# Performance work log

Hardware: AMD Instinct MI355X
Metric: run time of the kernel (lower is better)

## Reference

```python
import jax, jax.numpy as jnp
import numpy as np
from jax import lax


def _xavier(key, shape):
    fan_out, fan_in = shape
    lim = float(np.sqrt(6.0 / (fan_in + fan_out)))
    return jax.random.uniform(key, shape, jnp.float32, -lim, lim)


def setup_inputs() -> dict:
    V, E, H, F, B = 32000, 512, 256, 256, 64
    key = jax.random.key(0)
    ks = jax.random.split(key, 16)
    emb = _xavier(ks[0], (V, E)).at[0].set(0.0)  # padding_idx=0 zeroed
    return {
        'enc_feat': jax.random.normal(ks[1], (B, F), jnp.float32),
        'emb': emb,
        'Wh': _xavier(ks[2], (H, F)), 'bh': jnp.zeros((H,), jnp.float32),
        'Wc': _xavier(ks[3], (H, F)), 'bc': jnp.zeros((H,), jnp.float32),
        'Wih0': _xavier(ks[4], (4 * H, E)), 'Whh0': _xavier(ks[5], (4 * H, H)),
        'bih0': jnp.zeros((4 * H,), jnp.float32), 'bhh0': jnp.zeros((4 * H,), jnp.float32),
        'Wih1': _xavier(ks[6], (4 * H, H)), 'Whh1': _xavier(ks[7], (4 * H, H)),
        'bih1': jnp.zeros((4 * H,), jnp.float32), 'bhh1': jnp.zeros((4 * H,), jnp.float32),
        'Wout': _xavier(ks[8], (V, H)), 'bout': jnp.zeros((V,), jnp.float32),
        'sos_id': 1, 'eos_id': 2, 'max_len': 48,
    }


def _lstm_cell(x, h, c, Wih, Whh, bih, bhh):
    # PyTorch gate order: i, f, g, o
    g = x @ Wih.T + h @ Whh.T + (bih + bhh)
    i, f, gg, o = jnp.split(g, 4, axis=-1)
    c_new = jax.nn.sigmoid(f) * c + jax.nn.sigmoid(i) * jnp.tanh(gg)
    h_new = jax.nn.sigmoid(o) * jnp.tanh(c_new)
    return h_new, c_new


def reference(enc_feat, emb, Wh, bh, Wc, bc, Wih0, Whh0, bih0, bhh0,
              Wih1, Whh1, bih1, bhh1, Wout, bout, sos_id, eos_id, max_len):
    B = enc_feat.shape[0]
    h_init = enc_feat @ Wh.T + bh  # [B, H], repeated over num_layers
    c_init = enc_feat @ Wc.T + bc
    tok0 = jnp.full((B,), sos_id, jnp.int32)
    carry0 = (tok0, h_init, c_init, h_init, c_init,
              jnp.zeros((B,), bool), jnp.array(False))

    def step(carry, _):
        tok, h0, c0, h1, c1, done, all_done = carry
        x = emb[tok]                                   # [B, E]
        h0, c0 = _lstm_cell(x, h0, c0, Wih0, Whh0, bih0, bhh0)
        h1, c1 = _lstm_cell(h0, h1, c1, Wih1, Whh1, bih1, bhh1)
        logits = h1 @ Wout.T + bout                    # [B, V]
        nt = jnp.argmax(logits, axis=-1).astype(jnp.int32)  # greedy decode
        out = jnp.where(all_done, 0, nt)               # torch pads with 0 after break
        done = done | (out == eos_id)
        all_done = all_done | jnp.all(done)
        return (out, h0, c0, h1, c1, done, all_done), out

    _, toks = lax.scan(step, carry0, None, length=max_len)  # [max_len, B]
    return toks.T.astype(jnp.int64)  # [B, max_len]
```

## Files before the change

### kernel.cpp

```cpp
#include <hip/hip_runtime.h>
#include <math.h>

#define TSTEPS 48
#define NCELL 32
#define ND 224
#define NBLK (NCELL + ND)

#define OFF_W0T   0
#define OFF_W1T   524288
#define OFF_WH0T  786432
#define OFF_WH1T  1048576
#define OFF_BS0   1310720
#define OFF_BS1   1311744
#define OFF_HINIT 1312768
#define OFF_CINIT 1329152
#define OFF_H0BUF 1345536
#define OFF_H1BUF 1361920
#define OFF_FLOAT_END 1378304

#define FSTR 32
#define FL_H0F   0
#define FL_H1C   1024
#define FL_H1ALL 2048
#define FL_DFLAG 3072
#define FL_DMIR  10240
#define FL_TOK   11264
#define NFLAGU32 12288

typedef float f4v __attribute__((ext_vector_type(4)));

__device__ __forceinline__ unsigned ld_cohu(const unsigned* p) {
  return __hip_atomic_load((unsigned*)p, __ATOMIC_RELAXED, __HIP_MEMORY_SCOPE_AGENT);
}
__device__ __forceinline__ void st_cohu(unsigned* p, unsigned v) {
  __hip_atomic_store(p, v, __ATOMIC_RELAXED, __HIP_MEMORY_SCOPE_AGENT);
}
__device__ __forceinline__ unsigned long long ld_coh64(const unsigned long long* p) {
  return __hip_atomic_load((unsigned long long*)p, __ATOMIC_RELAXED, __HIP_MEMORY_SCOPE_AGENT);
}
__device__ __forceinline__ void st_coh64(unsigned long long* p, unsigned long long v) {
  __hip_atomic_store(p, v, __ATOMIC_RELAXED, __HIP_MEMORY_SCOPE_AGENT);
}
__device__ __forceinline__ float4 ldg_coh_f4(const float4* p) {
  f4v r;
  asm volatile("global_load_dwordx4 %0, %1, off sc0 sc1\n\ts_waitcnt vmcnt(0)"
               : "=v"(r) : "v"(p) : "memory");
  return make_float4(r.x, r.y, r.z, r.w);
}
__device__ __forceinline__ void ldg_coh_f4x4(const float4* p0, const float4* p1,
                                             const float4* p2, const float4* p3,
                                             float4& a, float4& b, float4& c, float4& d) {
  f4v ra, rb, rc, rd;
  asm volatile(
      "global_load_dwordx4 %0, %4, off sc0 sc1\n\t"
      "global_load_dwordx4 %1, %5, off sc0 sc1\n\t"
      "global_load_dwordx4 %2, %6, off sc0 sc1\n\t"
      "global_load_dwordx4 %3, %7, off sc0 sc1\n\t"
      "s_waitcnt vmcnt(0)"
      : "=&v"(ra), "=&v"(rb), "=&v"(rc), "=&v"(rd)
      : "v"(p0), "v"(p1), "v"(p2), "v"(p3) : "memory");
  a = make_float4(ra.x, ra.y, ra.z, ra.w);
  b = make_float4(rb.x, rb.y, rb.z, rb.w);
  c = make_float4(rc.x, rc.y, rc.z, rc.w);
  d = make_float4(rd.x, rd.y, rd.z, rd.w);
}
__device__ __forceinline__ void stg_coh_f4(float4* p, float4 v) {
  f4v t = {v.x, v.y, v.z, v.w};
  asm volatile("global_store_dwordx4 %0, %1, off sc0 sc1" :: "v"(p), "v"(t) : "memory");
}
__device__ __forceinline__ void drain_vm() {
  asm volatile("s_waitcnt vmcnt(0)" ::: "memory");
}
__device__ __forceinline__ float4 ldnt_f4(const float4* p) {
  f4v v = __builtin_nontemporal_load((const f4v*)p);
  return make_float4(v.x, v.y, v.z, v.w);
}
__device__ __forceinline__ float sigf(float x) { return 1.0f / (1.0f + expf(-x)); }
__device__ __forceinline__ unsigned long long u64max(unsigned long long a, unsigned long long b) {
  return a > b ? a : b;
}
__device__ __forceinline__ unsigned long long wmax64(unsigned long long k) {
#pragma unroll
  for (int off = 1; off < 64; off <<= 1) {
    unsigned long long o = __shfl_xor(k, off, 64);
    k = u64max(k, o);
  }
  return k;
}
__device__ __forceinline__ unsigned long long packkey(float lg, int v) {
  unsigned u = __float_as_uint(lg);
  u = (u & 0x80000000u) ? ~u : (u | 0x80000000u);
  return ((unsigned long long)u << 32) | (unsigned)(~(unsigned)v);
}
__device__ __forceinline__ float4 f4add(float4 a, float4 b) {
  return make_float4(a.x + b.x, a.y + b.y, a.z + b.z, a.w + b.w);
}

__global__ void lstm_init_kernel(const float* enc, const float* Wh, const float* bh,
                                 const float* Wc, const float* bc,
                                 const float* bih0, const float* bhh0,
                                 const float* bih1, const float* bhh1,
                                 float* ws, unsigned long long* key2, unsigned* flags) {
  const int tid = threadIdx.x, blk = blockIdx.x;
  if (blk < 64) {
    __shared__ float el[256];
    el[tid] = enc[blk * 256 + tid];
    __syncthreads();
    const float4* el4 = (const float4*)el;
    const float4* wh4 = (const float4*)(Wh + tid * 256);
    const float4* wc4 = (const float4*)(Wc + tid * 256);
    float ah = bh[tid], ac = bc[tid];
#pragma unroll 4
    for (int f = 0; f < 64; ++f) {
      float4 x = el4[f], a = wh4[f], b = wc4[f];
      ah = fmaf(a.x, x.x, fmaf(a.y, x.y, fmaf(a.z, x.z, fmaf(a.w, x.w, ah))));
      ac = fmaf(b.x, x.x, fmaf(b.y, x.y, fmaf(b.z, x.z, fmaf(b.w, x.w, ac))));
    }
    ws[OFF_HINIT + blk * 256 + tid] = ah;
    ws[OFF_CINIT + blk * 256 + tid] = ac;
  } else if (blk == 64) {
    for (int g = tid; g < 1024; g += 256) {
      int hh = g >> 9, gc = g & 511;
      int row = (gc >> 7) * 256 + hh * 128 + (gc & 127);
      ws[OFF_BS0 + g] = bih0[row] + bhh0[row];
      ws[OFF_BS1 + g] = bih1[row] + bhh1[row];
    }
  } else {
    const int base = (blk - 65) * 256 + tid;
    for (int i = base; i < 64 * 256; i += 15 * 256) key2[i] = 0ull;
    for (int i = base; i < NFLAGU32; i += 15 * 256) flags[i] = 0u;
  }
}

__global__ void lstm_relayout_kernel(const float* Wih0, const float* Whh0,
                                     const float* Wih1, const float* Whh1, float* ws) {
  const int gid = blockIdx.x * 256 + threadIdx.x;
  const int gstr = 256 * 256;
  const float* srcs[4] = {Wih0, Wih1, Whh0, Whh1};
  const int dsts[4] = {OFF_W0T, OFF_W1T, OFF_WH0T, OFF_WH1T};
  const int k4tot[4] = {128, 64, 64, 64};
  for (int s = 0; s < 4; ++s) {
    const int n = 2 * k4tot[s] * 512;
    float4* dst = (float4*)(ws + dsts[s]);
    const float4* src = (const float4*)srcs[s];
    for (int e = gid; e < n; e += gstr) {
      int hh = e / (k4tot[s] * 512);
      int r = e - hh * k4tot[s] * 512;
      int k4 = r / 512, gc = r - k4 * 512;
      int row = (gc >> 7) * 256 + hh * 128 + (gc & 127);
      dst[e] = src[(size_t)row * k4tot[s] + k4];
    }
  }
}

struct CellSm {
  float x[4 * 512];
  float4 part[1024];
  float4 r0res[512];
  float4 r1res[512];
  float h0[4 * 256];
  float h1[4 * 256];
  float c0[4 * 128];
  float c1[4 * 128];
  int tok[4];
  unsigned fm[32];
  unsigned long long fred[16];
  int done4;
  int alldone;
};
struct DSm {
  float w[16 * 144 * 4];
  float h[64 * 68];
  unsigned long long kr[128];
  unsigned long long epi[16 * 64];
};
union Smem { CellSm c; DSm d; };

template <int K4H>
__device__ __forceinline__ void gemv_half(const float4* __restrict__ W,
                                          const float* __restrict__ xl, int xstride,
                                          float4* __restrict__ part, int tid) {
  const int kh = tid >> 9;
  float a0 = 0.f, a1 = 0.f, a2 = 0.f, a3 = 0.f;
  const float4* wp = W + (size_t)(kh * K4H) * 512 + (tid & 511);
  const float* x0 = xl + kh * K4H * 4;
#pragma unroll 8
  for (int i = 0; i < K4H; ++i) {
    float4 w = wp[(size_t)i * 512];
    float4 xa = *(const float4*)(x0 + i * 4);
    float4 xb = *(const float4*)(x0 + xstride + i * 4);
    float4 xc = *(const float4*)(x0 + 2 * xstride + i * 4);
    float4 xd = *(const float4*)(x0 + 3 * xstride + i * 4);
    a0 = fmaf(w.x, xa.x, fmaf(w.y, xa.y, fmaf(w.z, xa.z, fmaf(w.w, xa.w, a0))));
    a1 = fmaf(w.x, xb.x, fmaf(w.y, xb.y, fmaf(w.z, xb.z, fmaf(w.w, xb.w, a1))));
    a2 = fmaf(w.x, xc.x, fmaf(w.y, xc.y, fmaf(w.z, xc.z, fmaf(w.w, xc.w, a2))));
    a3 = fmaf(w.x, xd.x, fmaf(w.y, xd.y, fmaf(w.z, xd.z, fmaf(w.w, xd.w, a3))));
  }
  part[tid] = make_float4(a0, a1, a2, a3);
}

__device__ __forceinline__ void cellfold(const float4* part, const float4* rres,
                                         const float* bs, float* cst, float* hst,
                                         int hh, int tid) {
  if (tid < 512) {
    int jj = tid & 127, b = tid >> 7;
    float g[4];
#pragma unroll
    for (int q = 0; q < 4; ++q) {
      int gc = q * 128 + jj;
      g[q] = ((const float*)&part[gc])[b] + ((const float*)&part[512 + gc])[b] +
             ((const float*)&rres[gc])[b] + bs[gc];
    }
    float c = cst[b * 128 + jj];
    float cn = sigf(g[1]) * c + sigf(g[0]) * tanhf(g[2]);
    float hn = sigf(g[3]) * tanhf(cn);
    cst[b * 128 + jj] = cn;
    hst[b * 256 + hh * 128 + jj] = hn;
  }
}

__global__ __launch_bounds__(1024, 4) void lstm_decode_kernel(
    const float* __restrict__ emb, const float* __restrict__ Wout,
    const float* __restrict__ bout, const int* __restrict__ sosp,
    const int* __restrict__ eosp, float* __restrict__ ws,
    unsigned long long* __restrict__ key2, unsigned* __restrict__ flags,
    int* __restrict__ out) {
  const int tid = threadIdx.x;
  const int blk = blockIdx.x;
  __shared__ Smem sm;
  const int eos = *eosp;
  const int sos = *sosp;
  float4* h0b4 = (float4*)(ws + OFF_H0BUF);
  float4* h1b4 = (float4*)(ws + OFF_H1BUF);

  if (blk < NCELL) {
    const int bg = blk >> 1, hh = blk & 1, ph = 1 - hh;
    const float4* W0 = (const float4*)(ws + OFF_W0T) + (size_t)hh * 128 * 512;
    const float4* W1 = (const float4*)(ws + OFF_W1T) + (size_t)hh * 64 * 512;
    const float4* WH0 = (const float4*)(ws + OFF_WH0T) + (size_t)hh * 64 * 512;
    const float4* WH1 = (const float4*)(ws + OFF_WH1T) + (size_t)hh * 64 * 512;
    const float* bs0 = ws + OFF_BS0 + hh * 512;
    const float* bs1 = ws + OFF_BS1 + hh * 512;

    {
      int b = tid >> 8, k = tid & 255;
      float hv = ws[OFF_HINIT + (bg * 4 + b) * 256 + k];
      sm.c.h0[b * 256 + k] = hv;
      sm.c.h1[b * 256 + k] = hv;
    }
    if (tid < 512) {
      int b = tid >> 7, jj = tid & 127;
      float cv = ws[OFF_CINIT + (bg * 4 + b) * 256 + hh * 128 + jj];
      sm.c.c0[b * 128 + jj] = cv;
      sm.c.c1[b * 128 + jj] = cv;
    }
    if (tid < 4) sm.c.tok[tid] = sos;
    if (tid == 0) { sm.c.done4 = 0; sm.c.alldone = 0; }
    __syncthreads();
    gemv_half<32>(WH0, sm.c.h0, 256, sm.c.part, tid);
    __syncthreads();
    if (tid < 512) sm.c.r0res[tid] = f4add(sm.c.part[tid], sm.c.part[512 + tid]);
    __syncthreads();
    gemv_half<32>(WH1, sm.c.h1, 256, sm.c.part, tid);
    __syncthreads();
    if (tid < 512) sm.c.r1res[tid] = f4add(sm.c.part[tid], sm.c.part[512 + tid]);
    __syncthreads();

    for (int t = 0; t < TSTEPS; ++t) {
      const unsigned T = (unsigned)(t + 1);
      if (tid < 512) {
        int b = tid >> 7, j = tid & 127;
        ((float4*)sm.c.x)[b * 128 + j] = ((const float4*)emb)[(size_t)sm.c.tok[b] * 128 + j];
      }
      __syncthreads();
      gemv_half<64>(W0, sm.c.x, 512, sm.c.part, tid);
      __syncthreads();
      cellfold(sm.c.part, sm.c.r0res, bs0, sm.c.c0, sm.c.h0, hh, tid);
      __syncthreads();
      if (tid < 128) {
        int b = tid >> 5, j = tid & 31;
        float4 v = *(float4*)&sm.c.h0[b * 256 + hh * 128 + j * 4];
        stg_coh_f4(h0b4 + (bg * 4 + b) * 64 + hh * 32 + j, v);
      }
      drain_vm();
      __syncthreads();
      if (tid == 0) {
        st_cohu(flags + FL_H0F + blk * FSTR, T);
        while (ld_cohu(flags + FL_H0F + (blk ^ 1) * FSTR) < T) __builtin_amdgcn_s_sleep(1);
      }
      __syncthreads();
      if (tid < 128) {
        int b = tid >> 5, j = tid & 31;
        float4 v = ldg_coh_f4(h0b4 + (bg * 4 + b) * 64 + ph * 32 + j);
        *(float4*)&sm.c.h0[b * 256 + ph * 128 + j * 4] = v;
      }
      __syncthreads();
      gemv_half<32>(W1, sm.c.h0, 256, sm.c.part, tid);
      __syncthreads();
      cellfold(sm.c.part, sm.c.r1res, bs1, sm.c.c1, sm.c.h1, hh, tid);
      __syncthreads();
      if (tid < 128) {
        int b = tid >> 5, j = tid & 31;
        float4 v = *(float4*)&sm.c.h1[b * 256 + hh * 128 + j * 4];
        stg_coh_f4(h1b4 + (bg * 4 + b) * 64 + hh * 32 + j, v);
      }
      drain_vm();
      __syncthreads();
      if (tid == 0) {
        st_cohu(flags + FL_H1C + blk * FSTR, T);
        while (ld_cohu(flags + FL_H1C + (blk ^ 1) * FSTR) < T) __builtin_amdgcn_s_sleep(1);
      }
      __syncthreads();
      if (tid < 128) {
        int b = tid >> 5, j = tid & 31;
        float4 v = ldg_coh_f4(h1b4 + (bg * 4 + b) * 64 + ph * 32 + j);
        *(float4*)&sm.c.h1[b * 256 + ph * 128 + j * 4] = v;
      }
      __syncthreads();
      if (t > 0) {
        if (tid < 64) {
          unsigned tgt = (unsigned)t << 8;
          unsigned got = tgt;
          for (;;) {
            if (tid < 32) got = ld_cohu(flags + FL_TOK + tid * FSTR);
            if (__all((int)(got >= tgt))) break;
            __builtin_amdgcn_s_sleep(2);
          }
          if (tid < 32) sm.c.fm[tid] = got & 0xFFu;
        }
        __syncthreads();
        if (tid < 64) {
          int ok = 1;
          if (tid < 32) ok = (sm.c.fm[tid] == 0xFu);
          int all = __all(ok);
          if (tid == 0) sm.c.alldone = all;
        }
        __syncthreads();
      }
      gemv_half<32>(WH0, sm.c.h0, 256, sm.c.part, tid);
      __syncthreads();
      if (tid < 512) sm.c.r0res[tid] = f4add(sm.c.part[tid], sm.c.part[512 + tid]);
      __syncthreads();
      gemv_half<32>(WH1, sm.c.h1, 256, sm.c.part, tid);
      __syncthreads();
      if (tid < 512) sm.c.r1res[tid] = f4add(sm.c.part[tid], sm.c.part[512 + tid]);
      __syncthreads();
      if (tid < 64) {
        unsigned v = T;
        for (;;) {
          if (tid < 7) v = ld_cohu(flags + FL_DFLAG + (blk * 7 + tid) * FSTR);
          if (__all((int)(v >= T))) break;
          __builtin_amdgcn_s_sleep(4);
        }
      }
      __syncthreads();
      if (tid == 0) st_cohu(flags + FL_DMIR + blk * FSTR, T);
      if (tid < 64) {
        unsigned v = T;
        for (;;) {
          if (tid < 32) v = ld_cohu(flags + FL_DMIR + tid * FSTR);
          if (__all((int)(v >= T))) break;
          __builtin_amdgcn_s_sleep(2);
        }
      }
      __syncthreads();
      {
        int bb = tid >> 8, i = tid & 255;
        unsigned long long k = ld_coh64(key2 + (size_t)(bg * 4 + bb) * 256 + i);
        k = wmax64(k);
        if ((tid & 63) == 0) sm.c.fred[tid >> 6] = k;
      }
      __syncthreads();
      if (tid < 4) {
        int bb = tid;
        unsigned long long m = u64max(u64max(sm.c.fred[bb * 4], sm.c.fred[bb * 4 + 1]),
                                      u64max(sm.c.fred[bb * 4 + 2], sm.c.fred[bb * 4 + 3]));
        int v = (int)(~(unsigned)m);
        int outv = sm.c.alldone ? 0 : v;
        out[(bg * 4 + bb) * TSTEPS + t] = outv;
        int nd = ((sm.c.done4 >> bb) & 1) | (outv == eos ? 1 : 0);
        sm.c.tok[bb] = outv;
        sm.c.fm[bb] = (unsigned)nd;
      }
      __syncthreads();
      if (tid == 0) {
        int mask = (int)(sm.c.fm[0] | (sm.c.fm[1] << 1) | (sm.c.fm[2] << 2) | (sm.c.fm[3] << 3));
        sm.c.done4 = mask;
        if (t < TSTEPS - 1)
          st_cohu(flags + FL_TOK + blk * FSTR, ((unsigned)(t + 1) << 8) | (unsigned)mask);
      }
      __syncthreads();
    }
  } else {
    const int d = blk - NCELL;
    const int r0 = (d * 32000) / ND, r1 = ((d + 1) * 32000) / ND;
    const int rows = r1 - r0, nep = rows - 128;
    const int bg = tid >> 7, v = tid & 127;
    const int erow = tid >> 6, eb = tid & 63;
    const float4* Wout4 = (const float4*)Wout;
    const int nq = 144 * 16;

    for (int t = 0; t < TSTEPS; ++t) {
      const unsigned T = (unsigned)(t + 1);
      float4 wpre[3];
#pragma unroll
      for (int p = 0; p < 3; ++p) {
        int e = tid + p * 1024;
        if (e < nq) {
          int j = e / 144, r = e - j * 144;
          int rc = r0 + r; if (rc > 31999) rc = 31999;
          wpre[p] = ldnt_f4(Wout4 + (size_t)rc * 64 + j);
        } else wpre[p] = make_float4(0.f, 0.f, 0.f, 0.f);
      }
#pragma unroll
      for (int p = 0; p < 3; ++p) {
        int e = tid + p * 1024;
        if (e < nq) {
          int j = e / 144, r = e - j * 144;
          *(float4*)&sm.d.w[(j * 144 + r) * 4] = wpre[p];
        }
      }
      if (tid < 64) {
        unsigned hv = T;
        for (;;) {
          if (tid < 32) hv = ld_cohu(flags + FL_H1C + tid * FSTR);
          if (__all((int)(hv >= T))) break;
          __builtin_amdgcn_s_sleep(4);
        }
      }
      __syncthreads();
      float4 hpre[4];
      {
        int b = tid >> 4, j = tid & 15;
        const float4* hp = (const float4*)h1b4 + (size_t)b * 64 + j;
        ldg_coh_f4x4(hp, hp + 16, hp + 32, hp + 48, hpre[0], hpre[1], hpre[2], hpre[3]);
      }
      float acc[8];
#pragma unroll
      for (int i = 0; i < 8; ++i) acc[i] = 0.f;
      float eacc = 0.f;

      for (int kc = 0; kc < 4; ++kc) {
        if (kc > 0) {
          __syncthreads();
#pragma unroll
          for (int p = 0; p < 3; ++p) {
            int e = tid + p * 1024;
            if (e < nq) {
              int j = e / 144, r = e - j * 144;
              *(float4*)&sm.d.w[(j * 144 + r) * 4] = wpre[p];
            }
          }
        }
        {
          int b = tid >> 4, j = tid & 15;
          *(float4*)&sm.d.h[b * 68 + j * 4] = hpre[kc];
        }
        __syncthreads();
        if (kc < 3) {
#pragma unroll
          for (int p = 0; p < 3; ++p) {
            int e = tid + p * 1024;
            if (e < nq) {
              int j = e / 144, r = e - j * 144;
              int rc = r0 + r; if (rc > 31999) rc = 31999;
              wpre[p] = ldnt_f4(Wout4 + (size_t)rc * 64 + (kc + 1) * 16 + j);
            }
          }
        }
#pragma unroll 4
        for (int k4 = 0; k4 < 16; ++k4) {
          float4 w4 = *(const float4*)&sm.d.w[(k4 * 144 + v) * 4];
#pragma unroll
          for (int bi = 0; bi < 8; ++bi) {
            float4 h4 = *(const float4*)&sm.d.h[(bg * 8 + bi) * 68 + k4 * 4];
            acc[bi] = fmaf(w4.x, h4.x, fmaf(w4.y, h4.y, fmaf(w4.z, h4.z, fmaf(w4.w, h4.w, acc[bi]))));
          }
        }
        if (erow < nep) {
#pragma unroll 4
          for (int k4 = 0; k4 < 16; ++k4) {
            float4 w4 = *(const float4*)&sm.d.w[(k4 * 144 + 128 + erow) * 4];
            float4 h4 = *(const float4*)&sm.d.h[eb * 68 + k4 * 4];
            eacc = fmaf(w4.x, h4.x, fmaf(w4.y, h4.y, fmaf(w4.z, h4.z, fmaf(w4.w, h4.w, eacc))));
          }
        }
      }
      {
        float bb_ = bout[r0 + v];
#pragma unroll
        for (int bi = 0; bi < 8; ++bi) {
          unsigned long long k = packkey(acc[bi] + bb_, r0 + v);
          k = wmax64(k);
          if ((tid & 63) == 0) sm.d.kr[(bg * 8 + bi) * 2 + (v >> 6)] = k;
        }
      }
      if (erow < nep) {
        sm.d.epi[erow * 64 + eb] = packkey(eacc + bout[r0 + 128 + erow], r0 + 128 + erow);
      } else {
        sm.d.epi[erow * 64 + eb] = 0ull;
      }
      __syncthreads();
      if (tid < 64) {
        unsigned long long m = u64max(sm.d.kr[tid * 2], sm.d.kr[tid * 2 + 1]);
#pragma unroll
        for (int er = 0; er < 15; ++er) m = u64max(m, sm.d.epi[er * 64 + tid]);
        st_coh64(key2 + (size_t)tid * 256 + d, m);
      }
      drain_vm();
      __syncthreads();
      if (tid == 0) st_cohu(flags + FL_DFLAG + d * FSTR, T);
    }
  }
}

extern "C" void kernel_launch(void* const* d_in, const int* in_sizes, int n_in,
                              void* d_out, int out_size, void* d_ws, size_t ws_size,
                              hipStream_t stream) {
  const float* enc  = (const float*)d_in[0];
  const float* emb  = (const float*)d_in[1];
  const float* Wh   = (const float*)d_in[2];
  const float* bh   = (const float*)d_in[3];
  const float* Wc   = (const float*)d_in[4];
  const float* bc   = (const float*)d_in[5];
  const float* Wih0 = (const float*)d_in[6];
  const float* Whh0 = (const float*)d_in[7];
  const float* bih0 = (const float*)d_in[8];
  const float* bhh0 = (const float*)d_in[9];
  const float* Wih1 = (const float*)d_in[10];
  const float* Whh1 = (const float*)d_in[11];
  const float* bih1 = (const float*)d_in[12];
  const float* bhh1 = (const float*)d_in[13];
  const float* Wout = (const float*)d_in[14];
  const float* bout = (const float*)d_in[15];
  const int* sosp   = (const int*)d_in[16];
  const int* eosp   = (const int*)d_in[17];

  float* ws = (float*)d_ws;
  char* base = (char*)d_ws + (size_t)OFF_FLOAT_END * 4;
  unsigned long long* key2 = (unsigned long long*)base;
  unsigned* flags          = (unsigned*)(base + 131072);
  int* out = (int*)d_out;

  lstm_init_kernel<<<80, 256, 0, stream>>>(enc, Wh, bh, Wc, bc, bih0, bhh0,
                                           bih1, bhh1, ws, key2, flags);
  lstm_relayout_kernel<<<256, 256, 0, stream>>>(Wih0, Whh0, Wih1, Whh1, ws);
  lstm_decode_kernel<<<NBLK, 1024, 0, stream>>>(emb, Wout, bout, sosp, eosp,
                                                ws, key2, flags, out);
}
```

Before: 3.375 ms.

## Remap output-projection threads to 32 rows x 2 batches and fuse argmax reduction

Reassigns work in the vocabulary-projection blocks so each thread computes 4 main rows plus one extra row for two batch entries, instead of one row for 8 batches plus a separate extra-row pass. The extra rows are folded into the main k-loop and each lane max-reduces its own rows before a 32-lane shuffle reduction, which removes the epilogue shared buffer and the serial 15-way max. Bias loads are hoisted out of the timestep loop. Each thread now does five weight LDS reads per k4 against two h reads, and register pressure from the fully unrolled kc loop may rise.

New measurement: 4.828 ms. 1.43x slower.

```diff
diff --git a/kernel.cpp b/kernel.cpp
--- a/kernel.cpp
+++ b/kernel.cpp
@@ -171,8 +171,7 @@
 struct DSm {
   float w[16 * 144 * 4];
   float h[64 * 68];
-  unsigned long long kr[128];
-  unsigned long long epi[16 * 64];
+  unsigned long long kr[64];
 };
 union Smem { CellSm c; DSm d; };
 
@@ -395,10 +394,14 @@
     const int d = blk - NCELL;
     const int r0 = (d * 32000) / ND, r1 = ((d + 1) * 32000) / ND;
     const int rows = r1 - r0, nep = rows - 128;
-    const int bg = tid >> 7, v = tid & 127;
-    const int erow = tid >> 6, eb = tid & 63;
+    const int v = tid & 31, bp = tid >> 5;
     const float4* Wout4 = (const float4*)Wout;
     const int nq = 144 * 16;
+
+    float bbm[4];
+#pragma unroll
+    for (int rs = 0; rs < 4; ++rs) bbm[rs] = bout[r0 + rs * 32 + v];
+    const float bbE = (v < nep) ? bout[r0 + 128 + v] : 0.f;
 
     for (int t = 0; t < TSTEPS; ++t) {
       const unsigned T = (unsigned)(t + 1);
@@ -435,11 +438,12 @@
         const float4* hp = (const float4*)h1b4 + (size_t)b * 64 + j;
         ldg_coh_f4x4(hp, hp + 16, hp + 32, hp + 48, hpre[0], hpre[1], hpre[2], hpre[3]);
       }
-      float acc[8];
-#pragma unroll
-      for (int i = 0; i < 8; ++i) acc[i] = 0.f;
-      float eacc = 0.f;
-
+      float accA[4], accB[4];
+      float eaA = 0.f, eaB = 0.f;
+#pragma unroll
+      for (int i = 0; i < 4; ++i) { accA[i] = 0.f; accB[i] = 0.f; }
+
+#pragma unroll
       for (int kc = 0; kc < 4; ++kc) {
         if (kc > 0) {
           __syncthreads();
@@ -470,43 +474,51 @@
         }
 #pragma unroll 4
         for (int k4 = 0; k4 < 16; ++k4) {
-          float4 w4 = *(const float4*)&sm.d.w[(k4 * 144 + v) * 4];
-#pragma unroll
-          for (int bi = 0; bi < 8; ++bi) {
-            float4 h4 = *(const float4*)&sm.d.h[(bg * 8 + bi) * 68 + k4 * 4];
-            acc[bi] = fmaf(w4.x, h4.x, fmaf(w4.y, h4.y, fmaf(w4.z, h4.z, fmaf(w4.w, h4.w, acc[bi]))));
+          const float* wb = &sm.d.w[(k4 * 144) * 4];
+          float4 w0 = *(const float4*)&wb[v * 4];
+          float4 w1 = *(const float4*)&wb[(32 + v) * 4];
+          float4 w2 = *(const float4*)&wb[(64 + v) * 4];
+          float4 w3 = *(const float4*)&wb[(96 + v) * 4];
+          float4 hA = *(const float4*)&sm.d.h[(2 * bp) * 68 + k4 * 4];
+          float4 hB = *(const float4*)&sm.d.h[(2 * bp + 1) * 68 + k4 * 4];
+          accA[0] = fmaf(w0.x, hA.x, fmaf(w0.y, hA.y, fmaf(w0.z, hA.z, fmaf(w0.w, hA.w, accA[0]))));
+          accB[0] = fmaf(w0.x, hB.x, fmaf(w0.y, hB.y, fmaf(w0.z, hB.z, fmaf(w0.w, hB.w, accB[0]))));
+          accA[1] = fmaf(w1.x, hA.x, fmaf(w1.y, hA.y, fmaf(w1.z, hA.z, fmaf(w1.w, hA.w, accA[1]))));
+          accB[1] = fmaf(w1.x, hB.x, fmaf(w1.y, hB.y, fmaf(w1.z, hB.z, fmaf(w1.w, hB.w, accB[1]))));
+          accA[2] = fmaf(w2.x, hA.x, fmaf(w2.y, hA.y, fmaf(w2.z, hA.z, fmaf(w2.w, hA.w, accA[2]))));
+          accB[2] = fmaf(w2.x, hB.x, fmaf(w2.y, hB.y, fmaf(w2.z, hB.z, fmaf(w2.w, hB.w, accB[2]))));
+          accA[3] = fmaf(w3.x, hA.x, fmaf(w3.y, hA.y, fmaf(w3.z, hA.z, fmaf(w3.w, hA.w, accA[3]))));
+          accB[3] = fmaf(w3.x, hB.x, fmaf(w3.y, hB.y, fmaf(w3.z, hB.z, fmaf(w3.w, hB.w, accB[3]))));
+          if (v < nep) {
+            float4 wE = *(const float4*)&wb[(128 + v) * 4];
+            eaA = fmaf(wE.x, hA.x, fmaf(wE.y, hA.y, fmaf(wE.z, hA.z, fmaf(wE.w, hA.w, eaA))));
+            eaB = fmaf(wE.x, hB.x, fmaf(wE.y, hB.y, fmaf(wE.z, hB.z, fmaf(wE.w, hB.w, eaB))));
           }
         }
-        if (erow < nep) {
-#pragma unroll 4
-          for (int k4 = 0; k4 < 16; ++k4) {
-            float4 w4 = *(const float4*)&sm.d.w[(k4 * 144 + 128 + erow) * 4];
-            float4 h4 = *(const float4*)&sm.d.h[eb * 68 + k4 * 4];
-            eacc = fmaf(w4.x, h4.x, fmaf(w4.y, h4.y, fmaf(w4.z, h4.z, fmaf(w4.w, h4.w, eacc))));
-          }
-        }
-      }
-      {
-        float bb_ = bout[r0 + v];
-#pragma unroll
-        for (int bi = 0; bi < 8; ++bi) {
-          unsigned long long k = packkey(acc[bi] + bb_, r0 + v);
-          k = wmax64(k);
-          if ((tid & 63) == 0) sm.d.kr[(bg * 8 + bi) * 2 + (v >> 6)] = k;
-        }
-      }
-      if (erow < nep) {
-        sm.d.epi[erow * 64 + eb] = packkey(eacc + bout[r0 + 128 + erow], r0 + 128 + erow);
-      } else {
-        sm.d.epi[erow * 64 + eb] = 0ull;
-      }
-      __syncthreads();
-      if (tid < 64) {
-        unsigned long long m = u64max(sm.d.kr[tid * 2], sm.d.kr[tid * 2 + 1]);
-#pragma unroll
-        for (int er = 0; er < 15; ++er) m = u64max(m, sm.d.epi[er * 64 + tid]);
-        st_coh64(key2 + (size_t)tid * 256 + d, m);
-      }
+      }
+      unsigned long long kA = packkey(accA[0] + bbm[0], r0 + v);
+      kA = u64max(kA, packkey(accA[1] + bbm[1], r0 + 32 + v));
+      kA = u64max(kA, packkey(accA[2] + bbm[2], r0 + 64 + v));
+      kA = u64max(kA, packkey(accA[3] + bbm[3], r0 + 96 + v));
+      unsigned long long kB = packkey(accB[0] + bbm[0], r0 + v);
+      kB = u64max(kB, packkey(accB[1] + bbm[1], r0 + 32 + v));
+      kB = u64max(kB, packkey(accB[2] + bbm[2], r0 + 64 + v));
+      kB = u64max(kB, packkey(accB[3] + bbm[3], r0 + 96 + v));
+      if (v < nep) {
+        kA = u64max(kA, packkey(eaA + bbE, r0 + 128 + v));
+        kB = u64max(kB, packkey(eaB + bbE, r0 + 128 + v));
+      }
+#pragma unroll
+      for (int off = 1; off < 32; off <<= 1) {
+        kA = u64max(kA, __shfl_xor(kA, off, 64));
+        kB = u64max(kB, __shfl_xor(kB, off, 64));
+      }
+      if ((tid & 31) == 0) {
+        sm.d.kr[2 * bp] = kA;
+        sm.d.kr[2 * bp + 1] = kB;
+      }
+      __syncthreads();
+      if (tid < 64) st_coh64(key2 + (size_t)tid * 256 + d, sm.d.kr[tid]);
       drain_vm();
       __syncthreads();
       if (tid == 0) st_cohu(flags + FL_DFLAG + d * FSTR, T);
```
